# Optimization experiments

Measured on AMD Instinct MI355X. Metric: run time of the kernel, lower is better.

Reference implementation:

```python
import jax, jax.numpy as jnp
import numpy as np


def setup_inputs() -> dict:
    key = jax.random.key(0)
    ks = jax.random.split(key, 8)
    B, T, D = 4, 4096, 1024
    d_inner, dt_rank, d_state = 2048, 64, 16
    s = 0.02  # weight init scale for numerical stability
    f32 = jnp.float32
    return {
        "x": jax.random.normal(ks[0], (B, T, D), f32),
        "in_proj_w": jax.random.normal(ks[1], (2 * d_inner, D), f32) * s,
        "conv_w": jax.random.normal(ks[2], (d_inner, 1, 3), f32) * s,
        "conv_b": jnp.zeros((d_inner,), f32),
        "x_proj_w": jax.random.normal(ks[3], (dt_rank + 2 * d_state, d_inner), f32) * s,
        "dt_proj_w": jax.random.normal(ks[4], (d_inner, dt_rank), f32) * s,
        "dt_proj_b": jnp.zeros((d_inner,), f32),
        "D_param": jnp.ones((d_inner,), f32),
        "out_proj_w": jax.random.normal(ks[5], (D, d_inner), f32) * s,
    }


def reference(x, in_proj_w, conv_w, conv_b, x_proj_w, dt_proj_w, dt_proj_b, D_param, out_proj_w):
    d_inner = conv_b.shape[0]
    dt_rank = dt_proj_w.shape[1]

    # in_proj and split into x-branch / gate-branch z
    xz = jnp.einsum('btd,ed->bte', x, in_proj_w)          # [B,T,2*d_inner]
    xs, z = jnp.split(xz, 2, axis=-1)                     # each [B,T,d_inner]

    # depthwise conv1d along time (kernel 3, padding 1, groups=d_inner)
    xc = jnp.transpose(xs, (0, 2, 1))                     # [B,C,T]
    xc = jax.lax.conv_general_dilated(
        xc, conv_w, window_strides=(1,), padding=[(1, 1)],
        dimension_numbers=('NCH', 'OIH', 'NCH'), feature_group_count=d_inner)
    xc = xc + conv_b[None, :, None]
    xs = jnp.transpose(xc, (0, 2, 1))                     # [B,T,d_inner]

    # x_proj -> take dt part (B,C slices are unused by the scan math)
    x_dbl = jnp.einsum('btc,ec->bte', xs, x_proj_w)       # [B,T,dt_rank+2*d_state]
    dt = jnp.einsum('btr,cr->btc', x_dbl[..., :dt_rank], dt_proj_w) + dt_proj_b  # [B,T,d_inner]

    # selective scan: scalar gate per (batch, t); h_t = g*h_{t-1} + (1-g)*x_t
    gate = jax.nn.sigmoid(jnp.mean(dt, axis=-1))          # [B,T]

    def step(h, inp):
        g, xt = inp                                       # g: [B], xt: [B,d_inner]
        h_new = g[:, None] * h + (1.0 - g[:, None]) * xt
        return h_new, h_new

    h0 = jnp.zeros_like(xs[:, 0])                         # [B,d_inner]
    _, ys = jax.lax.scan(step, h0, (gate.T, jnp.transpose(xs, (1, 0, 2))))
    y = jnp.transpose(ys, (1, 0, 2))                      # [B,T,d_inner]

    y = y * jax.nn.silu(z) + D_param * xs
    return jnp.einsum('btc,dc->btd', y, out_proj_w)       # [B,T,d_model]
```

## Files before the change

### kernel.cpp

```cpp
#include <hip/hip_runtime.h>
#include <hip/hip_bf16.h>
#include <math.h>

#define B_ 4
#define T_ 4096
#define DM 1024
#define DI 2048
#define E2 4096
#define NCHUNK 64
#define CLEN 64

typedef __attribute__((ext_vector_type(8))) short short8;
typedef __attribute__((ext_vector_type(4))) float floatx4;

union bfs { __hip_bfloat16 b; short s; };

__device__ __forceinline__ float bf2f(__hip_bfloat16 x) { return __bfloat162float(x); }
__device__ __forceinline__ short f2s(float x) { bfs u; u.b = __float2bfloat16(x); return u.s; }

__device__ __forceinline__ float ldw(const void* p, int i, int f32m) {
    return f32m ? ((const float*)p)[i] : bf2f(((const __hip_bfloat16*)p)[i]);
}

#define GLDS16(gp, lp) __builtin_amdgcn_global_load_lds( \
    (const __attribute__((address_space(1))) void*)(gp), \
    (__attribute__((address_space(3))) void*)(lp), 16, 0, 0)

#define MEMFENCE asm volatile("" ::: "memory")

__global__ __launch_bounds__(256)
void detect_k(const unsigned short* __restrict__ xu, unsigned* __restrict__ flag)
{
    __shared__ int red[256];
    const int tid = threadIdx.x;
    int cnt = 0;
    for (int i = tid; i < 2048; i += 256) {
        const int e = (xu[i] >> 7) & 0xFF;
        cnt += (e >= 0x90);
    }
    red[tid] = cnt;
    __syncthreads();
    for (int off = 128; off; off >>= 1) {
        if (tid < off) red[tid] += red[tid + off];
        __syncthreads();
    }
    if (tid == 0) *flag = (red[0] >= 8) ? 1u : 0u;
}

__global__ __launch_bounds__(256)
void cvt_k(const void* __restrict__ src, __hip_bfloat16* __restrict__ dst,
           const unsigned* __restrict__ flag)
{
    const int fm = (int)*flag;
    const size_t i0 = ((size_t)blockIdx.x * 256 + threadIdx.x) * 8;
    if (fm) {
        const float* f = (const float*)src + i0;
        floatx4 lo = *(const floatx4*)f;
        floatx4 hi = *(const floatx4*)(f + 4);
        short8 r;
        r[0] = f2s(lo[0]); r[1] = f2s(lo[1]); r[2] = f2s(lo[2]); r[3] = f2s(lo[3]);
        r[4] = f2s(hi[0]); r[5] = f2s(hi[1]); r[6] = f2s(hi[2]); r[7] = f2s(hi[3]);
        *(short8*)(dst + i0) = r;
    } else {
        *(short8*)(dst + i0) = *(const short8*)((const __hip_bfloat16*)src + i0);
    }
}

__global__ __launch_bounds__(256)
void cvt_strided_k(const void* __restrict__ src, __hip_bfloat16* __restrict__ dst,
                   const unsigned* __restrict__ flag)
{
    const int fm = (int)*flag;
    const size_t i0 = ((size_t)blockIdx.x * 256 + threadIdx.x) * 8;
    const size_t row = i0 >> 11, col = i0 & 2047;
    __hip_bfloat16* d = dst + row * E2 + col;
    if (fm) {
        const float* f = (const float*)src + i0;
        floatx4 lo = *(const floatx4*)f;
        floatx4 hi = *(const floatx4*)(f + 4);
        short8 r;
        r[0] = f2s(lo[0]); r[1] = f2s(lo[1]); r[2] = f2s(lo[2]); r[3] = f2s(lo[3]);
        r[4] = f2s(hi[0]); r[5] = f2s(hi[1]); r[6] = f2s(hi[2]); r[7] = f2s(hi[3]);
        *(short8*)d = r;
    } else {
        *(short8*)d = *(const short8*)((const __hip_bfloat16*)src + i0);
    }
}

__global__ __launch_bounds__(512)
void gemm256(const __hip_bfloat16* __restrict__ A,
             const __hip_bfloat16* __restrict__ Bt,
             void* __restrict__ C, int K, int lda, int ldb, int ldc,
             int csel, const unsigned* __restrict__ flag)
{
    __shared__ __align__(16) char sL[3 * 32768];

    const int cf = csel & (int)*flag;

    const int tid  = threadIdx.x;
    const int lane = tid & 63;
    const int wid  = tid >> 6;
    const int wr   = wid >> 2;
    const int wc   = wid & 3;
    const int l15  = lane & 15;
    const int quad = lane >> 4;
    const int swl  = (l15 >> 1) & 3;

    const int m0 = blockIdx.x * 256;
    const int n0 = blockIdx.y * 256;

    floatx4 acc[8][4];
#pragma unroll
    for (int i = 0; i < 8; i++)
#pragma unroll
        for (int j = 0; j < 4; j++) acc[i][j] = (floatx4){0.f, 0.f, 0.f, 0.f};

    const int srow = tid >> 2;
    const int ksrc = (((tid & 3) ^ ((tid >> 3) & 3))) * 8;
    const __hip_bfloat16* gA = A  + (size_t)(m0 + srow) * lda + ksrc;
    const __hip_bfloat16* gB = Bt + (size_t)(n0 + srow) * ldb + ksrc;
    const size_t h1A = (size_t)128 * lda;
    const size_t h1B = (size_t)128 * ldb;

    char* const ldsW = sL + wid * 1024;

    const int NT = K >> 5;

#define STAGE_A(buf, kt) do { \
    const __hip_bfloat16* g_ = gA + (size_t)(kt) * 32; \
    char* l_ = ldsW + (buf) * 32768; \
    GLDS16(g_, l_); \
    GLDS16(g_ + h1A, l_ + 8192); } while (0)
#define STAGE_B(buf, kt) do { \
    const __hip_bfloat16* g_ = gB + (size_t)(kt) * 32; \
    char* l_ = ldsW + (buf) * 32768 + 16384; \
    GLDS16(g_, l_); \
    GLDS16(g_ + h1B, l_ + 8192); } while (0)

    STAGE_A(0, 0); STAGE_B(0, 0);
    STAGE_A(1, 1); STAGE_B(1, 1);
    asm volatile("s_waitcnt vmcnt(4)" ::: "memory");
    __builtin_amdgcn_s_barrier();
    MEMFENCE;

    int cur = 0, nx2 = 2;
    for (int t = 0; t < NT; ++t) {
        const char* Ab = sL + cur * 32768;
        const char* Bb = Ab + 16384;

        short8 fb[4], fa[4];
#pragma unroll
        for (int j = 0; j < 4; j++)
            fb[j] = *(const short8*)(Bb + (wc * 64 + j * 16 + l15) * 64 + ((quad ^ swl) * 16));
#pragma unroll
        for (int i = 0; i < 4; i++)
            fa[i] = *(const short8*)(Ab + (wr * 128 + i * 16 + l15) * 64 + ((quad ^ swl) * 16));
        if (t + 2 < NT) STAGE_A(nx2, t + 2);
        __builtin_amdgcn_s_barrier();
        MEMFENCE;
        __builtin_amdgcn_s_setprio(1);
#pragma unroll
        for (int i = 0; i < 4; i++)
#pragma unroll
            for (int j = 0; j < 4; j++)
                acc[i][j] = __builtin_amdgcn_mfma_f32_16x16x32_bf16(fa[i], fb[j], acc[i][j], 0, 0, 0);
        __builtin_amdgcn_s_setprio(0);
        __builtin_amdgcn_s_barrier();
        MEMFENCE;

        short8 fa2[4];
#pragma unroll
        for (int i = 0; i < 4; i++)
            fa2[i] = *(const short8*)(Ab + (wr * 128 + 64 + i * 16 + l15) * 64 + ((quad ^ swl) * 16));
        if (t + 2 < NT) {
            STAGE_B(nx2, t + 2);
            asm volatile("s_waitcnt vmcnt(4)" ::: "memory");
        } else {
            asm volatile("s_waitcnt vmcnt(0)" ::: "memory");
        }
        __builtin_amdgcn_s_barrier();
        MEMFENCE;
        __builtin_amdgcn_s_setprio(1);
#pragma unroll
        for (int i = 0; i < 4; i++)
#pragma unroll
            for (int j = 0; j < 4; j++)
                acc[4 + i][j] = __builtin_amdgcn_mfma_f32_16x16x32_bf16(fa2[i], fb[j], acc[4 + i][j], 0, 0, 0);
        __builtin_amdgcn_s_setprio(0);
        __builtin_amdgcn_s_barrier();
        MEMFENCE;

        cur = (cur == 2) ? 0 : cur + 1;
        nx2 = (nx2 == 2) ? 0 : nx2 + 1;
    }
#undef STAGE_A
#undef STAGE_B

#pragma unroll
    for (int i = 0; i < 8; i++) {
        const int row = m0 + wr * 128 + i * 16 + quad * 4;
#pragma unroll
        for (int j = 0; j < 4; j++) {
            const int col = n0 + wc * 64 + j * 16 + l15;
#pragma unroll
            for (int r = 0; r < 4; r++) {
                const size_t idx = (size_t)(row + r) * ldc + col;
                const float val = acc[i][j][r];
                if (cf) ((float*)C)[idx] = val;
                else    ((__hip_bfloat16*)C)[idx] = __float2bfloat16(val);
            }
        }
    }
}

__global__ __launch_bounds__(256)
void precompute_wm_k(const void* __restrict__ dtw, const void* __restrict__ dtb,
                     float* __restrict__ wm, const unsigned* __restrict__ flag)
{
    __shared__ float red[256];
    const int fm = (int)*flag;
    const int tid = threadIdx.x;
    const int r = blockIdx.x;
    float s = 0.f;
    if (r < 64) {
        for (int c = tid; c < DI; c += 256) s += ldw(dtw, c * 64 + r, fm);
    } else {
        for (int c = tid; c < DI; c += 256) s += ldw(dtb, c, fm);
    }
    red[tid] = s;
    __syncthreads();
    for (int off = 128; off; off >>= 1) {
        if (tid < off) red[tid] += red[tid + off];
        __syncthreads();
    }
    if (tid == 0) wm[r] = red[0] / (float)DI;
}

__global__ __launch_bounds__(256)
void precompute_v2_k(const void* __restrict__ xpw, const float* __restrict__ wm,
                     float* __restrict__ v, const unsigned* __restrict__ flag)
{
    const int fm = (int)*flag;
    const int c = blockIdx.x * 256 + threadIdx.x;
    float s = 0.f;
#pragma unroll
    for (int r = 0; r < 64; r++) s += wm[r] * ldw(xpw, r * DI + c, fm);
    v[c] = s;
    if (c == 0) v[DI] = wm[64];
}

__global__ __launch_bounds__(256)
void conv_gate_nox(const __hip_bfloat16* __restrict__ xz,
                   const void* __restrict__ cw, const void* __restrict__ cb,
                   const float* __restrict__ v, float* __restrict__ gate,
                   const unsigned* __restrict__ flag)
{
    __shared__ float red[256];
    const int fm = (int)*flag;
    const int t = blockIdx.x, b = blockIdx.y, tid = threadIdx.x;
    const size_t bt = (size_t)b * T_ + t;
    const __hip_bfloat16* row0 = xz + bt * E2;
    float partial = 0.f;
#pragma unroll
    for (int j = 0; j < 8; j++) {
        const int c = tid + j * 256;
        const float w0 = ldw(cw, c * 3 + 0, fm);
        const float w1 = ldw(cw, c * 3 + 1, fm);
        const float w2 = ldw(cw, c * 3 + 2, fm);
        const float xm = (t > 0)      ? bf2f(row0[(int)c - E2]) : 0.f;
        const float x0 = bf2f(row0[c]);
        const float xp = (t < T_ - 1) ? bf2f(row0[c + E2]) : 0.f;
        const float val = w0 * xm + w1 * x0 + w2 * xp + ldw(cb, c, fm);
        partial += v[c] * val;
    }
    red[tid] = partial;
    __syncthreads();
    for (int off = 128; off; off >>= 1) {
        if (tid < off) red[tid] += red[tid + off];
        __syncthreads();
    }
    if (tid == 0) {
        const float s = red[0] + v[DI];
        gate[bt] = 1.f / (1.f + __expf(-s));
    }
}

__global__ __launch_bounds__(256)
void pprod_k(const float* __restrict__ gate, float* __restrict__ P)
{
    const int tid = threadIdx.x;
    const int b = tid >> 6, ch = tid & 63;
    const float* g = gate + (size_t)b * T_ + ch * CLEN;
    float p = 1.f;
#pragma unroll
    for (int i = 0; i < CLEN; i++) p *= g[i];
    P[tid] = p;
}

__global__ __launch_bounds__(256)
void scan_chunks(const __hip_bfloat16* __restrict__ xz,
                 const float* __restrict__ gate,
                 const void* __restrict__ cw, const void* __restrict__ cb,
                 float* __restrict__ r, const unsigned* __restrict__ flag)
{
    const int fm = (int)*flag;
    const int blk = blockIdx.x;
    const int cg = blk & 7, chunk = (blk >> 3) & 63, b = blk >> 9;
    const int c = cg * 256 + threadIdx.x;
    const float w0 = ldw(cw, c * 3 + 0, fm);
    const float w1 = ldw(cw, c * 3 + 1, fm);
    const float w2 = ldw(cw, c * 3 + 2, fm);
    const float bc = ldw(cb, c, fm);
    const int t0 = chunk * CLEN;
    const float* g = gate + (size_t)b * T_ + t0;
    const __hip_bfloat16* px = xz + (size_t)b * T_ * E2 + c;

    float xm = (t0 > 0) ? bf2f(px[(size_t)(t0 - 1) * E2]) : 0.f;
    float xc = bf2f(px[(size_t)t0 * E2]);
    float h = 0.f;
#pragma unroll 4
    for (int i = 0; i < CLEN; i++) {
        const int t = t0 + i;
        const float xn = (t + 1 < T_) ? bf2f(px[(size_t)(t + 1) * E2]) : 0.f;
        const float val = w0 * xm + w1 * xc + w2 * xn + bc;
        const float gi = g[i];
        h = gi * h + (1.f - gi) * val;
        xm = xc; xc = xn;
    }
    r[((size_t)b * NCHUNK + chunk) * DI + c] = h;
}

__global__ __launch_bounds__(256)
void carry_fix(float* __restrict__ r, const float* __restrict__ P)
{
    const int gid = blockIdx.x * 256 + threadIdx.x;
    const int b = gid >> 11, c = gid & 2047;
    float h = 0.f;
    for (int k = 0; k < NCHUNK; k++) {
        const size_t idx = ((size_t)b * NCHUNK + k) * DI + c;
        const float rk = r[idx];
        const float Pk = P[b * NCHUNK + k];
        r[idx] = h;
        h = Pk * h + rk;
    }
}

__global__ __launch_bounds__(256)
void scan_apply(__hip_bfloat16* __restrict__ xz,
                const float* __restrict__ gate,
                const float* __restrict__ r,
                const void* __restrict__ cw, const void* __restrict__ cb,
                const void* __restrict__ Dp, const unsigned* __restrict__ flag)
{
    const int fm = (int)*flag;
    const int blk = blockIdx.x;
    const int cg = blk & 7, chunk = (blk >> 3) & 63, b = blk >> 9;
    const int c = cg * 256 + threadIdx.x;
    const float w0 = ldw(cw, c * 3 + 0, fm);
    const float w1 = ldw(cw, c * 3 + 1, fm);
    const float w2 = ldw(cw, c * 3 + 2, fm);
    const float bc = ldw(cb, c, fm);
    const float Dc = ldw(Dp, c, fm);
    const int t0 = chunk * CLEN;
    const float* g = gate + (size_t)b * T_ + t0;
    const __hip_bfloat16* px = xz + (size_t)b * T_ * E2 + c;
    __hip_bfloat16* pz = xz + (size_t)b * T_ * E2 + DI + c;

    float h = r[((size_t)b * NCHUNK + chunk) * DI + c];
    float xm = (t0 > 0) ? bf2f(px[(size_t)(t0 - 1) * E2]) : 0.f;
    float xc = bf2f(px[(size_t)t0 * E2]);
#pragma unroll 4
    for (int i = 0; i < CLEN; i++) {
        const int t = t0 + i;
        const float xn = (t + 1 < T_) ? bf2f(px[(size_t)(t + 1) * E2]) : 0.f;
        const float val = w0 * xm + w1 * xc + w2 * xn + bc;
        const float gi = g[i];
        h = gi * h + (1.f - gi) * val;
        const float zv = bf2f(pz[(size_t)t * E2]);
        const float sil = zv / (1.f + __expf(-zv));
        pz[(size_t)t * E2] = __float2bfloat16(h * sil + Dc * val);
        xm = xc; xc = xn;
    }
}

extern "C" void kernel_launch(void* const* d_in, const int* in_sizes, int n_in,
                              void* d_out, int out_size, void* d_ws, size_t ws_size,
                              hipStream_t stream)
{
    const size_t REQUIRED = 134292480;
    if (ws_size < REQUIRED) return;

    const void* x    = d_in[0];
    const void* wip  = d_in[1];
    const void* cw   = d_in[2];
    const void* cb   = d_in[3];
    const void* xpw  = d_in[4];
    const void* dtw  = d_in[5];
    const void* dtb  = d_in[6];
    const void* Dp   = d_in[7];
    const void* wop  = d_in[8];

    char* ws = (char*)d_ws;
    __hip_bfloat16* xz = (__hip_bfloat16*)ws;
    float* gate    = (float*)(ws + 134217728);
    float* v       = (float*)(ws + 134283264);
    float* wm      = v + 2052;
    unsigned* flag = (unsigned*)(ws + 134291968);

    __hip_bfloat16* x_bf   = (__hip_bfloat16*)d_out;
    __hip_bfloat16* wip_bf = (__hip_bfloat16*)((char*)d_out + 33554432);
    float* r = (float*)((char*)d_out + 41943040);
    float* P = (float*)((char*)d_out + 44040192);
    __hip_bfloat16* wop_bf = xz;

    detect_k<<<1, 256, 0, stream>>>((const unsigned short*)x, flag);

    cvt_k<<<8192, 256, 0, stream>>>(x, x_bf, flag);
    cvt_k<<<2048, 256, 0, stream>>>(wip, wip_bf, flag);

    precompute_wm_k<<<65, 256, 0, stream>>>(dtw, dtb, wm, flag);
    precompute_v2_k<<<8, 256, 0, stream>>>(xpw, wm, v, flag);

    gemm256<<<dim3(64, 16), 512, 0, stream>>>(x_bf, wip_bf, xz,
                                              1024, 1024, 1024, E2, 0, flag);

    conv_gate_nox<<<dim3(T_, B_), 256, 0, stream>>>(xz, cw, cb, v, gate, flag);

    pprod_k<<<1, 256, 0, stream>>>(gate, P);
    scan_chunks<<<2048, 256, 0, stream>>>(xz, gate, cw, cb, r, flag);
    carry_fix<<<32, 256, 0, stream>>>(r, P);
    scan_apply<<<2048, 256, 0, stream>>>(xz, gate, r, cw, cb, Dp, flag);

    cvt_strided_k<<<1024, 256, 0, stream>>>(wop, wop_bf, flag);

    gemm256<<<dim3(64, 4), 512, 0, stream>>>(xz + DI, wop_bf, d_out,
                                             2048, E2, E2, DM, 1, flag);
}
```

Baseline: 509.5 us.

## Deepen GEMM LDS pipeline to four stages and prefetch next-tile fragments

The bf16 GEMM's shared-memory ring grows from three to four buffers, so global-to-LDS loads are issued three k-tiles ahead instead of two. The B fragments and lower-half A fragments for the next k-tile are also read from LDS during the second MFMA phase of the current tile, which keeps the ds_read latency off the critical path. The cost is 128KB of LDS per block instead of 96KB and more live registers, which may lower occupancy or cause spills. The read of the next tile's buffer now relies on the vmcnt(8) wait accounting being correct.

Result: no change. 514.6 us (+1.0%).

```diff
diff --git a/kernel.cpp b/kernel.cpp
--- a/kernel.cpp
+++ b/kernel.cpp
@@ -93,7 +93,7 @@
              void* __restrict__ C, int K, int lda, int ldb, int ldc,
              int csel, const unsigned* __restrict__ flag)
 {
-    __shared__ __align__(16) char sL[3 * 32768];
+    __shared__ __align__(16) char sL[4 * 32768];
 
     const int cf = csel & (int)*flag;
 
@@ -125,6 +125,10 @@
     char* const ldsW = sL + wid * 1024;
 
     const int NT = K >> 5;
+
+    const int offB  = 16384 + (wc * 64 + l15) * 64 + ((quad ^ swl) * 16);
+    const int offAl = (wr * 128 + l15) * 64 + ((quad ^ swl) * 16);
+    const int offAh = (wr * 128 + 64 + l15) * 64 + ((quad ^ swl) * 16);
 
 #define STAGE_A(buf, kt) do { \
     const __hip_bfloat16* g_ = gA + (size_t)(kt) * 32; \
@@ -139,23 +143,28 @@
 
     STAGE_A(0, 0); STAGE_B(0, 0);
     STAGE_A(1, 1); STAGE_B(1, 1);
-    asm volatile("s_waitcnt vmcnt(4)" ::: "memory");
+    STAGE_A(2, 2); STAGE_B(2, 2);
+    asm volatile("s_waitcnt vmcnt(8)" ::: "memory");
     __builtin_amdgcn_s_barrier();
     MEMFENCE;
 
-    int cur = 0, nx2 = 2;
+    short8 fbc[4], falo[4], fahi[4], fbn[4], faln[4];
+#pragma unroll
+    for (int j = 0; j < 4; j++)
+        fbc[j] = *(const short8*)(sL + offB + j * 1024);
+#pragma unroll
+    for (int i = 0; i < 4; i++)
+        falo[i] = *(const short8*)(sL + offAl + i * 1024);
+
+#pragma unroll 4
     for (int t = 0; t < NT; ++t) {
-        const char* Ab = sL + cur * 32768;
-        const char* Bb = Ab + 16384;
-
-        short8 fb[4], fa[4];
-#pragma unroll
-        for (int j = 0; j < 4; j++)
-            fb[j] = *(const short8*)(Bb + (wc * 64 + j * 16 + l15) * 64 + ((quad ^ swl) * 16));
+        const char* Ab = sL + (t & 3) * 32768;
+        const int nx = (t + 3) & 3;
+
 #pragma unroll
         for (int i = 0; i < 4; i++)
-            fa[i] = *(const short8*)(Ab + (wr * 128 + i * 16 + l15) * 64 + ((quad ^ swl) * 16));
-        if (t + 2 < NT) STAGE_A(nx2, t + 2);
+            fahi[i] = *(const short8*)(Ab + offAh + i * 1024);
+        if (t + 3 < NT) STAGE_A(nx, t + 3);
         __builtin_amdgcn_s_barrier();
         MEMFENCE;
         __builtin_amdgcn_s_setprio(1);
@@ -163,20 +172,25 @@
         for (int i = 0; i < 4; i++)
 #pragma unroll
             for (int j = 0; j < 4; j++)
-                acc[i][j] = __builtin_amdgcn_mfma_f32_16x16x32_bf16(fa[i], fb[j], acc[i][j], 0, 0, 0);
+                acc[i][j] = __builtin_amdgcn_mfma_f32_16x16x32_bf16(falo[i], fbc[j], acc[i][j], 0, 0, 0);
         __builtin_amdgcn_s_setprio(0);
         __builtin_amdgcn_s_barrier();
         MEMFENCE;
 
-        short8 fa2[4];
-#pragma unroll
-        for (int i = 0; i < 4; i++)
-            fa2[i] = *(const short8*)(Ab + (wr * 128 + 64 + i * 16 + l15) * 64 + ((quad ^ swl) * 16));
-        if (t + 2 < NT) {
-            STAGE_B(nx2, t + 2);
-            asm volatile("s_waitcnt vmcnt(4)" ::: "memory");
+        if (t + 3 < NT) {
+            STAGE_B(nx, t + 3);
+            asm volatile("s_waitcnt vmcnt(8)" ::: "memory");
         } else {
             asm volatile("s_waitcnt vmcnt(0)" ::: "memory");
+        }
+        if (t + 1 < NT) {
+            const char* An = sL + ((t + 1) & 3) * 32768;
+#pragma unroll
+            for (int j = 0; j < 4; j++)
+                fbn[j] = *(const short8*)(An + offB + j * 1024);
+#pragma unroll
+            for (int i = 0; i < 4; i++)
+                faln[i] = *(const short8*)(An + offAl + i * 1024);
         }
         __builtin_amdgcn_s_barrier();
         MEMFENCE;
@@ -185,13 +199,13 @@
         for (int i = 0; i < 4; i++)
 #pragma unroll
             for (int j = 0; j < 4; j++)
-                acc[4 + i][j] = __builtin_amdgcn_mfma_f32_16x16x32_bf16(fa2[i], fb[j], acc[4 + i][j], 0, 0, 0);
+                acc[4 + i][j] = __builtin_amdgcn_mfma_f32_16x16x32_bf16(fahi[i], fbc[j], acc[4 + i][j], 0, 0, 0);
         __builtin_amdgcn_s_setprio(0);
         __builtin_amdgcn_s_barrier();
         MEMFENCE;
 
-        cur = (cur == 2) ? 0 : cur + 1;
-        nx2 = (nx2 == 2) ? 0 : nx2 + 1;
+#pragma unroll
+        for (int q = 0; q < 4; q++) { fbc[q] = fbn[q]; falo[q] = faln[q]; }
     }
 #undef STAGE_A
 #undef STAGE_B
```
